# Optimization experiments

Measured on AMD Instinct MI355X. Metric: run time of the kernel, lower is better.

The kernel has to match this reference:

```python
import jax, jax.numpy as jnp
import numpy as np

B, T, D, H = 4, 1024, 1024, 16
DK = D // H
SCALE = float(np.sqrt(DK))


def setup_inputs() -> dict:
    key = jax.random.key(0)
    ks = jax.random.split(key, 12)
    std = 1.0 / np.sqrt(D)
    inp = {
        "x": jax.random.normal(ks[0], (B, T, D), dtype=jnp.float32),
        "s2_distances": jax.random.uniform(ks[1], (B, T, T), dtype=jnp.float32),
        # causal mask: 1 where attention allowed (j <= i)
        "mask": jnp.broadcast_to(jnp.tril(jnp.ones((T, T), dtype=jnp.int32)), (B, T, T)),
        "Wq": jax.random.uniform(ks[2], (D, D), jnp.float32, -std, std),
        "bq": jax.random.uniform(ks[3], (D,), jnp.float32, -std, std),
        "Wk": jax.random.uniform(ks[4], (D, D), jnp.float32, -std, std),
        "bk": jax.random.uniform(ks[5], (D,), jnp.float32, -std, std),
        "Wv": jax.random.uniform(ks[6], (D, D), jnp.float32, -std, std),
        "bv": jax.random.uniform(ks[7], (D,), jnp.float32, -std, std),
        "Wo": jax.random.uniform(ks[8], (D, D), jnp.float32, -std, std),
        "bo": jax.random.uniform(ks[9], (D,), jnp.float32, -std, std),
        "spatial_weight": jnp.float32(0.5),
    }
    return inp


def reference(x, s2_distances, mask, Wq, bq, Wk, bk, Wv, bv, Wo, bo, spatial_weight):
    b, t, _ = x.shape
    # projections: torch nn.Linear is x @ W.T + b
    def proj(W, bias):
        y = jnp.einsum("btd,ed->bte", x, W) + bias
        return y.reshape(b, t, H, DK).transpose(0, 2, 1, 3)  # [B,H,T,dk]

    Q, K, V = proj(Wq, bq), proj(Wk, bk), proj(Wv, bv)
    # scores: QK^T/sqrt(dk) - |alpha| * dist  (dist broadcast over heads)
    scores = jnp.einsum("bhqd,bhkd->bhqk", Q, K) / SCALE
    scores = scores - jnp.abs(spatial_weight) * s2_distances[:, None, :, :]
    scores = jnp.where(mask[:, None, :, :] == 0, -jnp.inf, scores)
    probs = jax.nn.softmax(scores, axis=-1)
    out = jnp.einsum("bhqk,bhkd->bhqd", probs, V)
    out = out.transpose(0, 2, 1, 3).reshape(b, t, D)
    return jnp.einsum("btd,ed->bte", out, Wo) + bo
```

## Files before the change

### kernel.cpp

```cpp
#include <hip/hip_runtime.h>
#include <stdint.h>

#define Tt 1024
#define Dd 1024
#define Hh 16

typedef unsigned short u16;
typedef __attribute__((ext_vector_type(8))) short short8;
typedef __attribute__((ext_vector_type(4))) float f32x4;
typedef __attribute__((ext_vector_type(4))) unsigned short u16x4;

typedef const __attribute__((address_space(1))) uint32_t* gptr_t;
typedef __attribute__((address_space(3))) uint32_t* lptr_t;

#define QSCALE 0.18033688011112042f
#define LOG2E 1.4426950408889634f

static __device__ __forceinline__ u16 f2bf(float f) {
  union { float f; unsigned u; } x;
  x.f = f;
  unsigned u = x.u;
  return (u16)((u + 0x7fffu + ((u >> 16) & 1u)) >> 16);
}

static __device__ __forceinline__ u16 f2bf_fast(float f) {
  union { float f; unsigned u; } x;
  x.f = f;
  return (u16)((x.u + 0x8000u) >> 16);
}

static __device__ __forceinline__ float fexp2(float x) {
#if __has_builtin(__builtin_amdgcn_exp2f)
  return __builtin_amdgcn_exp2f(x);
#else
  return exp2f(x);
#endif
}

__global__ __launch_bounds__(256) void cvt_kernel(
    const float* __restrict__ x, const float* __restrict__ wq,
    const float* __restrict__ wk, const float* __restrict__ wv,
    const float* __restrict__ wo, u16* __restrict__ xb, u16* __restrict__ wb) {
  size_t i = ((size_t)blockIdx.x * 256 + threadIdx.x) * 4;
  const size_t XN = (size_t)4 * 1024 * 1024;
  const float* src;
  u16* dst;
  size_t off;
  if (i < XN) {
    src = x; dst = xb; off = i;
  } else {
    size_t j = i - XN;
    int wi = (int)(j >> 20);
    src = (wi == 0) ? wq : (wi == 1) ? wk : (wi == 2) ? wv : wo;
    dst = wb + ((size_t)wi << 20);
    off = j & ((1u << 20) - 1);
  }
  float4 v = *(const float4*)(src + off);
  u16x4 o;
  o.x = f2bf(v.x); o.y = f2bf(v.y); o.z = f2bf(v.z); o.w = f2bf(v.w);
  *(u16x4*)(dst + off) = o;
}

static __device__ __forceinline__ void gemm_mainloop_db(
    const u16* __restrict__ A, const u16* __restrict__ W,
    u16* lds, int m0, int n0, f32x4 acc[2][4]) {
  const int t = threadIdx.x;
  const int w = t >> 6, l = t & 63;
  const int quad = l >> 4, l15 = l & 15;
  const int wm = (w >> 1) * 32, wn = (w & 1) * 64;
  const int srow = t >> 3;
  const int scol = ((l & 7) ^ ((l >> 3) & 7)) * 8;
  const u16* ga = A + (size_t)(m0 + srow) * Dd + scol;
  const u16* gb = W + (size_t)(n0 + srow) * Dd + scol;
  char* ldc = (char*)lds;
  const int xr = l15 & 7;

  auto stage = [&](int k0, int buf) {
    char* base = ldc + buf * 32768 + w * 1024;
#pragma unroll
    for (int i = 0; i < 2; i++) {
      __builtin_amdgcn_global_load_lds((gptr_t)(ga + k0 + (size_t)i * 64 * Dd),
                                       (lptr_t)(base + i * 8192), 16, 0, 0);
      __builtin_amdgcn_global_load_lds((gptr_t)(gb + k0 + (size_t)i * 64 * Dd),
                                       (lptr_t)(base + 16384 + i * 8192), 16, 0, 0);
    }
  };

  stage(0, 0);
#pragma unroll 1
  for (int it = 0; it < Dd / 64; it++) {
    const int buf = it & 1;
    __builtin_amdgcn_s_waitcnt(0);
    __syncthreads();
    if (it + 1 < Dd / 64) stage((it + 1) * 64, buf ^ 1);
    const u16* lA = lds + buf * 16384;
    const u16* lB = lA + 8192;
#pragma unroll
    for (int kk = 0; kk < 2; kk++) {
      short8 af[2], bfr[4];
#pragma unroll
      for (int mi = 0; mi < 2; mi++)
        af[mi] = *(const short8*)(lA + (wm + mi * 16 + l15) * 64 +
                                  (((kk * 4 + quad) ^ xr) * 8));
#pragma unroll
      for (int ni = 0; ni < 4; ni++)
        bfr[ni] = *(const short8*)(lB + (wn + ni * 16 + l15) * 64 +
                                   (((kk * 4 + quad) ^ xr) * 8));
#pragma unroll
      for (int mi = 0; mi < 2; mi++)
#pragma unroll
        for (int ni = 0; ni < 4; ni++)
          acc[mi][ni] = __builtin_amdgcn_mfma_f32_16x16x32_bf16(af[mi], bfr[ni], acc[mi][ni], 0, 0, 0);
    }
  }
}

__global__ __launch_bounds__(512) void gemm_qkv_kernel(
    const u16* __restrict__ xb, const u16* __restrict__ wb,
    const float* __restrict__ bq, const float* __restrict__ bk,
    const float* __restrict__ bv, u16* __restrict__ Q, u16* __restrict__ Kk,
    u16* __restrict__ Vt) {
  __shared__ u16 lds[2 * 16384];
  const int z = blockIdx.z;
  const u16* W = wb + ((size_t)z << 20);
  const float* bias = (z == 0) ? bq : (z == 1) ? bk : bv;
  const int m0 = blockIdx.x * 128, n0 = blockIdx.y * 128;
  f32x4 acc[2][4];
#pragma unroll
  for (int i = 0; i < 2; i++)
#pragma unroll
    for (int j = 0; j < 4; j++) acc[i][j] = (f32x4){0.f, 0.f, 0.f, 0.f};
  gemm_mainloop_db(xb, W, lds, m0, n0, acc);
  const int t = threadIdx.x, w = t >> 6, l = t & 63, quad = l >> 4, l15 = l & 15;
  const int wm = (w >> 1) * 32, wn = (w & 1) * 64;
  u16* smem = lds;
  __syncthreads();
  const float scl = (z == 0) ? QSCALE : 1.0f;
  if (z < 2) {
#pragma unroll
    for (int mi = 0; mi < 2; mi++)
#pragma unroll
      for (int ni = 0; ni < 4; ni++) {
        const int n = wn + ni * 16 + l15;
        const float bn = bias[n0 + n];
#pragma unroll
        for (int r = 0; r < 4; r++) {
          const int m = wm + mi * 16 + quad * 4 + r;
          smem[m * 128 + n] = f2bf((acc[mi][ni][r] + bn) * scl);
        }
      }
  } else {
#pragma unroll
    for (int mi = 0; mi < 2; mi++)
#pragma unroll
      for (int ni = 0; ni < 4; ni++) {
        const int n = wn + ni * 16 + l15;
        const float bn = bias[n0 + n];
        u16x4 o;
        o.x = f2bf(acc[mi][ni][0] + bn);
        o.y = f2bf(acc[mi][ni][1] + bn);
        o.z = f2bf(acc[mi][ni][2] + bn);
        o.w = f2bf(acc[mi][ni][3] + bn);
        *(u16x4*)&smem[n * 128 + wm + mi * 16 + quad * 4] = o;
      }
  }
  __syncthreads();
  const int row = t >> 4;
  const int col = (t & 15) * 8;
  if (z < 2) {
    u16* out = (z == 0) ? Q : Kk;
#pragma unroll
    for (int it = 0; it < 4; it++) {
      const int rr = it * 32 + row;
      *(short8*)(out + (size_t)(m0 + rr) * Dd + n0 + col) = *(const short8*)&smem[rr * 128 + col];
    }
  } else {
    const int b2 = m0 >> 10, tt0 = m0 & (Tt - 1);
#pragma unroll
    for (int it = 0; it < 4; it++) {
      const int rr = it * 32 + row;
      *(short8*)(Vt + ((size_t)b2 * Dd + n0 + rr) * Tt + tt0 + col) = *(const short8*)&smem[rr * 128 + col];
    }
  }
}

__global__ __launch_bounds__(512) void gemm_out_kernel(
    const u16* __restrict__ Ao, const u16* __restrict__ Wo,
    const float* __restrict__ bo, float* __restrict__ out) {
  __shared__ u16 lds[32768];
  const int mt = blockIdx.x & 31, ny = blockIdx.x >> 5;
  const int m0 = mt * 128, n0 = ny * 128;
  const int t = threadIdx.x, w = t >> 6, l = t & 63;
  const int quad = l >> 4, l15 = l & 15;
  const int wr = w >> 2, wn = w & 3;
  char* ldc = (char*)lds;

  const int srow = w * 8 + (l >> 3);
  const int schunk = ((l & 7) ^ ((l >> 3) & 7)) * 8;
  const u16* gA = Ao + (size_t)(m0 + srow) * Dd + schunk;
  const u16* gB = Wo + (size_t)(n0 + srow) * Dd + schunk;

  auto stage = [&](int kt) {
    char* base = ldc + (kt & 1) * 32768 + w * 1024;
#pragma unroll
    for (int i = 0; i < 2; i++) {
      __builtin_amdgcn_global_load_lds(
          (gptr_t)(gA + (size_t)i * 64 * Dd + (size_t)kt * 64),
          (lptr_t)(base + i * 8192), 16, 0, 0);
      __builtin_amdgcn_global_load_lds(
          (gptr_t)(gB + (size_t)i * 64 * Dd + (size_t)kt * 64),
          (lptr_t)(base + 16384 + i * 8192), 16, 0, 0);
    }
  };

  f32x4 acc[4][2];
#pragma unroll
  for (int i = 0; i < 4; i++)
#pragma unroll
    for (int j = 0; j < 2; j++) acc[i][j] = (f32x4){0.f, 0.f, 0.f, 0.f};

  stage(0); stage(1);
  asm volatile("s_waitcnt vmcnt(4)" ::: "memory");
  __builtin_amdgcn_s_barrier();

  const int swl = l15 & 7;

#pragma unroll 1
  for (int kt = 0; kt < 16; kt++) {
    const char* sl = ldc + (kt & 1) * 32768;
    short8 af[2][4], bfv[2][2];
#pragma unroll
    for (int ks = 0; ks < 2; ks++) {
      const int cs = ((ks * 4 + quad) ^ swl) * 16;
#pragma unroll
      for (int mi = 0; mi < 4; mi++)
        af[ks][mi] = *(const short8*)(sl + (wr * 64 + mi * 16 + l15) * 128 + cs);
#pragma unroll
      for (int ni = 0; ni < 2; ni++)
        bfv[ks][ni] = *(const short8*)(sl + 16384 + (wn * 32 + ni * 16 + l15) * 128 + cs);
    }
    __builtin_amdgcn_s_barrier();
    if (kt + 2 < 16) stage(kt + 2);
    asm volatile("s_waitcnt lgkmcnt(0)" ::: "memory");
    __builtin_amdgcn_sched_barrier(0);
    __builtin_amdgcn_s_setprio(1);
#pragma unroll
    for (int ks = 0; ks < 2; ks++)
#pragma unroll
      for (int mi = 0; mi < 4; mi++)
#pragma unroll
        for (int ni = 0; ni < 2; ni++)
          acc[mi][ni] = __builtin_amdgcn_mfma_f32_16x16x32_bf16(
              af[ks][mi], bfv[ks][ni], acc[mi][ni], 0, 0, 0);
    __builtin_amdgcn_s_setprio(0);
    if (kt < 14) {
      asm volatile("s_waitcnt vmcnt(4)" ::: "memory");
    } else if (kt == 14) {
      asm volatile("s_waitcnt vmcnt(0)" ::: "memory");
    }
    if (kt < 15) __builtin_amdgcn_s_barrier();
  }

#pragma unroll
  for (int mi = 0; mi < 4; mi++)
#pragma unroll
    for (int ni = 0; ni < 2; ni++) {
      const int n = n0 + wn * 32 + ni * 16 + l15;
      const float bn = bo[n];
#pragma unroll
      for (int r = 0; r < 4; r++) {
        const int m = m0 + wr * 64 + mi * 16 + quad * 4 + r;
        out[(size_t)m * Dd + n] = acc[mi][ni][r] + bn;
      }
    }
}

__global__ __launch_bounds__(256) void attn_kernel(
    const u16* __restrict__ Q, const u16* __restrict__ Kk,
    const u16* __restrict__ Vt, const float* __restrict__ dist,
    const float* __restrict__ alphap, u16* __restrict__ Oo) {
  __shared__ u16 lK[2][64 * 64];
  __shared__ u16 lV[2][64 * 64];
  __shared__ u16 lPp[4][16 * 64];
  const int t = threadIdx.x, w = t >> 6, l = t & 63, quad = l >> 4, l15 = l & 15;
  const int g = blockIdx.x >> 8;
  const int j = (blockIdx.x >> 6) & 3;
  const int bh = blockIdx.x & 63;
  const int qb = (g == 0) ? 15 - j : (g == 1) ? 8 + j : (g == 2) ? 7 - j : j;
  const int h = bh & (Hh - 1), b = bh >> 4;
  const int q0 = qb * 64;
  const float scl = -fabsf(alphap[0]) * LOG2E;

  const int srow = w * 8 + (l >> 3);
  const int schunk = ((l & 7) ^ ((l >> 3) & 7)) * 8;
  const u16* gK = Kk + ((size_t)b * Tt + srow) * Dd + h * 64 + schunk;
  const u16* gV = Vt + ((size_t)b * Dd + h * 64 + srow) * Tt + schunk;
  char* lKc0 = (char*)&lK[0][0];
  char* lVc0 = (char*)&lV[0][0];
  const int wbase = w * 1024;

  auto stage = [&](int k0, int buf) {
#pragma unroll
    for (int i = 0; i < 2; i++) {
      __builtin_amdgcn_global_load_lds(
          (gptr_t)(gK + (size_t)(k0 + i * 32) * Dd),
          (lptr_t)(lKc0 + buf * 8192 + wbase + i * 4096), 16, 0, 0);
      __builtin_amdgcn_global_load_lds(
          (gptr_t)(gV + (size_t)(i * 32) * Tt + k0),
          (lptr_t)(lVc0 + buf * 8192 + wbase + i * 4096), 16, 0, 0);
    }
  };

  const int qrow = q0 + w * 16 + l15;
  const u16* Qp = Q + ((size_t)b * Tt + qrow) * Dd + h * 64 + quad * 8;
  const short8 qf0 = *(const short8*)Qp;
  const short8 qf1 = *(const short8*)(Qp + 32);
  const float* bp = dist + ((size_t)b * Tt + qrow) * Tt + quad * 4;

  const int xr = l15 & 7;
  u16* lpr = &lPp[w][l15 * 64];
  const int niter = qb + 1;

  f32x4 oacc[4];
#pragma unroll
  for (int dt = 0; dt < 4; dt++) oacc[dt] = (f32x4){0.f, 0.f, 0.f, 0.f};
  f32x4 lsum4 = (f32x4){0.f, 0.f, 0.f, 0.f};
  f32x4 bbA[4], bbB[4], bbC[4];

  stage(0, 0);
#pragma unroll
  for (int nt = 0; nt < 4; nt++) bbA[nt] = *(const f32x4*)(bp + nt * 16);
  if (niter > 1) {
#pragma unroll
    for (int nt = 0; nt < 4; nt++) bbB[nt] = *(const f32x4*)(bp + 64 + nt * 16);
  } else {
#pragma unroll
    for (int nt = 0; nt < 4; nt++) bbB[nt] = bbA[nt];
  }

#pragma unroll 1
  for (int kt = 0; kt < niter; kt++) {
    const int buf = kt & 1;
    if (kt + 1 < niter) {
      asm volatile("s_waitcnt vmcnt(4)" ::: "memory");
    } else {
      asm volatile("s_waitcnt vmcnt(0)" ::: "memory");
    }
    __builtin_amdgcn_s_barrier();
    if (kt + 1 < niter) stage((kt + 1) * 64, buf ^ 1);
    if (kt + 2 < niter) {
#pragma unroll
      for (int nt = 0; nt < 4; nt++)
        bbC[nt] = *(const f32x4*)(bp + (kt + 2) * 64 + nt * 16);
    }
    f32x4 sacc[4];
#pragma unroll
    for (int nt = 0; nt < 4; nt++) {
#pragma unroll
      for (int r = 0; r < 4; r++) sacc[nt][r] = scl * bbA[nt][r];
    }
#pragma unroll
    for (int ks = 0; ks < 2; ks++) {
      const short8 qf = ks ? qf1 : qf0;
      const int cs = ((ks * 4 + quad) ^ xr) * 8;
#pragma unroll
      for (int nt = 0; nt < 4; nt++) {
        const short8 kf = *(const short8*)&lK[buf][(nt * 16 + l15) * 64 + cs];
        sacc[nt] = __builtin_amdgcn_mfma_f32_16x16x32_bf16(kf, qf, sacc[nt], 0, 0, 0);
      }
    }
    if (kt == qb) {
      const int kbase = kt * 64 + quad * 4;
#pragma unroll
      for (int nt = 0; nt < 4; nt++) {
        u16x4 pk;
#pragma unroll
        for (int r = 0; r < 4; r++) {
          const float p = (kbase + nt * 16 + r <= qrow) ? fexp2(sacc[nt][r]) : 0.f;
          lsum4[nt] += p;
          pk[r] = f2bf_fast(p);
        }
        *(u16x4*)&lpr[((nt * 4 + quad) ^ (xr << 1)) * 4] = pk;
      }
    } else {
#pragma unroll
      for (int nt = 0; nt < 4; nt++) {
        u16x4 pk;
#pragma unroll
        for (int r = 0; r < 4; r++) {
          const float p = fexp2(sacc[nt][r]);
          lsum4[nt] += p;
          pk[r] = f2bf_fast(p);
        }
        *(u16x4*)&lpr[((nt * 4 + quad) ^ (xr << 1)) * 4] = pk;
      }
    }
#pragma unroll
    for (int ks = 0; ks < 2; ks++) {
      const int cs = ((ks * 4 + quad) ^ xr) * 8;
      const short8 pa = *(const short8*)&lpr[cs];
#pragma unroll
      for (int dt = 0; dt < 4; dt++) {
        const short8 vf = *(const short8*)&lV[buf][(dt * 16 + l15) * 64 + cs];
        oacc[dt] = __builtin_amdgcn_mfma_f32_16x16x32_bf16(pa, vf, oacc[dt], 0, 0, 0);
      }
    }
#pragma unroll
    for (int nt = 0; nt < 4; nt++) { bbA[nt] = bbB[nt]; bbB[nt] = bbC[nt]; }
  }

  float lsum = (lsum4[0] + lsum4[1]) + (lsum4[2] + lsum4[3]);
  lsum += __shfl_xor(lsum, 16);
  lsum += __shfl_xor(lsum, 32);
  const float inv = 1.0f / lsum;
  float invq[4];
#pragma unroll
  for (int r = 0; r < 4; r++) invq[r] = __shfl(inv, quad * 4 + r);
#pragma unroll
  for (int dt = 0; dt < 4; dt++) {
#pragma unroll
    for (int r = 0; r < 4; r++) {
      Oo[((size_t)b * Tt + q0 + w * 16 + quad * 4 + r) * Dd + h * 64 + dt * 16 + l15] =
          f2bf(oacc[dt][r] * invq[r]);
    }
  }
}

extern "C" void kernel_launch(void* const* d_in, const int* in_sizes, int n_in,
                              void* d_out, int out_size, void* d_ws, size_t ws_size,
                              hipStream_t stream) {
  const float* x = (const float*)d_in[0];
  const float* dist = (const float*)d_in[1];
  const float* Wq = (const float*)d_in[3];
  const float* bq = (const float*)d_in[4];
  const float* Wk = (const float*)d_in[5];
  const float* bk = (const float*)d_in[6];
  const float* Wv = (const float*)d_in[7];
  const float* bv = (const float*)d_in[8];
  const float* Wo = (const float*)d_in[9];
  const float* bo = (const float*)d_in[10];
  const float* alphap = (const float*)d_in[11];

  char* ws = (char*)d_ws;
  u16* xb = (u16*)(ws);
  u16* wb = (u16*)(ws + ((size_t)8 << 20));
  u16* Qb = (u16*)(ws + ((size_t)16 << 20));
  u16* Kb = (u16*)(ws + ((size_t)24 << 20));
  u16* Vtb = (u16*)(ws + ((size_t)32 << 20));
  u16* Ob = xb;
  float* outp = (float*)d_out;

  cvt_kernel<<<8192, 256, 0, stream>>>(x, Wq, Wk, Wv, Wo, xb, wb);
  dim3 g1(32, 8, 3);
  gemm_qkv_kernel<<<g1, 512, 0, stream>>>(xb, wb, bq, bk, bv, Qb, Kb, Vtb);
  attn_kernel<<<1024, 256, 0, stream>>>(Qb, Kb, Vtb, dist, alphap, Ob);
  gemm_out_kernel<<<256, 512, 0, stream>>>(Ob, wb + ((size_t)3 << 20), bo, outp);
}
```

Baseline: 194.6 us.

## Software-pipeline QK^T of next tile with softmax and PV of current tile

```diff
diff --git a/kernel.cpp b/kernel.cpp
--- a/kernel.cpp
+++ b/kernel.cpp
@@ -299,16 +299,19 @@
   char* lVc0 = (char*)&lV[0][0];
   const int wbase = w * 1024;
 
-  auto stage = [&](int k0, int buf) {
-#pragma unroll
-    for (int i = 0; i < 2; i++) {
+  auto stageK = [&](int kt, int buf) {
+#pragma unroll
+    for (int i = 0; i < 2; i++)
       __builtin_amdgcn_global_load_lds(
-          (gptr_t)(gK + (size_t)(k0 + i * 32) * Dd),
+          (gptr_t)(gK + (size_t)(kt * 64 + i * 32) * Dd),
           (lptr_t)(lKc0 + buf * 8192 + wbase + i * 4096), 16, 0, 0);
+  };
+  auto stageV = [&](int kt, int buf) {
+#pragma unroll
+    for (int i = 0; i < 2; i++)
       __builtin_amdgcn_global_load_lds(
-          (gptr_t)(gV + (size_t)(i * 32) * Tt + k0),
+          (gptr_t)(gV + (size_t)(i * 32) * Tt + kt * 64),
           (lptr_t)(lVc0 + buf * 8192 + wbase + i * 4096), 16, 0, 0);
-    }
   };
 
   const int qrow = q0 + w * 16 + l15;
@@ -325,48 +328,65 @@
 #pragma unroll
   for (int dt = 0; dt < 4; dt++) oacc[dt] = (f32x4){0.f, 0.f, 0.f, 0.f};
   f32x4 lsum4 = (f32x4){0.f, 0.f, 0.f, 0.f};
-  f32x4 bbA[4], bbB[4], bbC[4];
-
-  stage(0, 0);
-#pragma unroll
-  for (int nt = 0; nt < 4; nt++) bbA[nt] = *(const f32x4*)(bp + nt * 16);
+  f32x4 sacc_A[4], bbA[4];
+
+  stageK(0, 0);
+  stageV(0, 0);
+  if (niter > 1) stageK(1, 1);
+  f32x4 bb0[4];
+#pragma unroll
+  for (int nt = 0; nt < 4; nt++) bb0[nt] = *(const f32x4*)(bp + nt * 16);
+  asm volatile("s_waitcnt vmcnt(0)" ::: "memory");
+  __builtin_amdgcn_s_barrier();
+#pragma unroll
+  for (int nt = 0; nt < 4; nt++) {
+#pragma unroll
+    for (int r = 0; r < 4; r++) sacc_A[nt][r] = scl * bb0[nt][r];
+  }
+#pragma unroll
+  for (int ks = 0; ks < 2; ks++) {
+    const short8 qf = ks ? qf1 : qf0;
+    const int cs = ((ks * 4 + quad) ^ xr) * 8;
+#pragma unroll
+    for (int nt = 0; nt < 4; nt++) {
+      const short8 kf = *(const short8*)&lK[0][(nt * 16 + l15) * 64 + cs];
+      sacc_A[nt] = __builtin_amdgcn_mfma_f32_16x16x32_bf16(kf, qf, sacc_A[nt], 0, 0, 0);
+    }
+  }
   if (niter > 1) {
 #pragma unroll
-    for (int nt = 0; nt < 4; nt++) bbB[nt] = *(const f32x4*)(bp + 64 + nt * 16);
-  } else {
-#pragma unroll
-    for (int nt = 0; nt < 4; nt++) bbB[nt] = bbA[nt];
-  }
+    for (int nt = 0; nt < 4; nt++) bbA[nt] = *(const f32x4*)(bp + 64 + nt * 16);
+  }
+  __builtin_amdgcn_s_barrier();
 
 #pragma unroll 1
   for (int kt = 0; kt < niter; kt++) {
     const int buf = kt & 1;
+    if (kt + 2 < niter) stageK(kt + 2, buf);
+    if (kt + 1 < niter) stageV(kt + 1, buf ^ 1);
+    __builtin_amdgcn_sched_barrier(0);
+    f32x4 bbB[4];
+    if (kt + 2 < niter) {
+#pragma unroll
+      for (int nt = 0; nt < 4; nt++)
+        bbB[nt] = *(const f32x4*)(bp + (kt + 2) * 64 + nt * 16);
+    }
+    f32x4 sacc_B[4];
     if (kt + 1 < niter) {
-      asm volatile("s_waitcnt vmcnt(4)" ::: "memory");
-    } else {
-      asm volatile("s_waitcnt vmcnt(0)" ::: "memory");
-    }
-    __builtin_amdgcn_s_barrier();
-    if (kt + 1 < niter) stage((kt + 1) * 64, buf ^ 1);
-    if (kt + 2 < niter) {
-#pragma unroll
-      for (int nt = 0; nt < 4; nt++)
-        bbC[nt] = *(const f32x4*)(bp + (kt + 2) * 64 + nt * 16);
-    }
-    f32x4 sacc[4];
-#pragma unroll
-    for (int nt = 0; nt < 4; nt++) {
-#pragma unroll
-      for (int r = 0; r < 4; r++) sacc[nt][r] = scl * bbA[nt][r];
-    }
-#pragma unroll
-    for (int ks = 0; ks < 2; ks++) {
-      const short8 qf = ks ? qf1 : qf0;
-      const int cs = ((ks * 4 + quad) ^ xr) * 8;
 #pragma unroll
       for (int nt = 0; nt < 4; nt++) {
-        const short8 kf = *(const short8*)&lK[buf][(nt * 16 + l15) * 64 + cs];
-        sacc[nt] = __builtin_amdgcn_mfma_f32_16x16x32_bf16(kf, qf, sacc[nt], 0, 0, 0);
+#pragma unroll
+        for (int r = 0; r < 4; r++) sacc_B[nt][r] = scl * bbA[nt][r];
+      }
+#pragma unroll
+      for (int ks = 0; ks < 2; ks++) {
+        const short8 qf = ks ? qf1 : qf0;
+        const int cs = ((ks * 4 + quad) ^ xr) * 8;
+#pragma unroll
+        for (int nt = 0; nt < 4; nt++) {
+          const short8 kf = *(const short8*)&lK[buf ^ 1][(nt * 16 + l15) * 64 + cs];
+          sacc_B[nt] = __builtin_amdgcn_mfma_f32_16x16x32_bf16(kf, qf, sacc_B[nt], 0, 0, 0);
+        }
       }
     }
     if (kt == qb) {
@@ -376,7 +396,7 @@
         u16x4 pk;
 #pragma unroll
         for (int r = 0; r < 4; r++) {
-          const float p = (kbase + nt * 16 + r <= qrow) ? fexp2(sacc[nt][r]) : 0.f;
+          const float p = (kbase + nt * 16 + r <= qrow) ? fexp2(sacc_A[nt][r]) : 0.f;
           lsum4[nt] += p;
           pk[r] = f2bf_fast(p);
         }
@@ -388,7 +408,7 @@
         u16x4 pk;
 #pragma unroll
         for (int r = 0; r < 4; r++) {
-          const float p = fexp2(sacc[nt][r]);
+          const float p = fexp2(sacc_A[nt][r]);
           lsum4[nt] += p;
           pk[r] = f2bf_fast(p);
         }
@@ -405,8 +425,16 @@
         oacc[dt] = __builtin_amdgcn_mfma_f32_16x16x32_bf16(pa, vf, oacc[dt], 0, 0, 0);
       }
     }
-#pragma unroll
-    for (int nt = 0; nt < 4; nt++) { bbA[nt] = bbB[nt]; bbB[nt] = bbC[nt]; }
+    if (kt + 1 < niter) {
+      if (kt + 2 < niter) {
+        asm volatile("s_waitcnt vmcnt(4)" ::: "memory");
+      } else {
+        asm volatile("s_waitcnt vmcnt(0)" ::: "memory");
+      }
+      __builtin_amdgcn_s_barrier();
+#pragma unroll
+      for (int nt = 0; nt < 4; nt++) { sacc_A[nt] = sacc_B[nt]; bbA[nt] = bbB[nt]; }
+    }
   }
 
   float lsum = (lsum4[0] + lsum4[1]) + (lsum4[2] + lsum4[3]);
```

New measurement: 198.5 us. 2.0% more time.
